# Kernel optimization log

Hardware: AMD Instinct MI355X
Metric: run time of the kernel (lower is better)

Reference implementation:

```python
import jax, jax.numpy as jnp
import numpy as np

MIN_TAU = 1e-3  # max(1e-5, config.CELL_MIN_TAU=0.001)
EPS_U = 1e-10   # guard for log(u) in gumbel transform


def setup_inputs() -> dict:
    key = jax.random.key(0)
    ks = jax.random.split(key, 6)
    B, I, H = 16, 1024, 2048
    x_t = jax.random.normal(ks[0], (B, I), dtype=jnp.float32)
    h_prev = jax.random.normal(ks[1], (B, H), dtype=jnp.float32)
    W_ih_w = jax.random.normal(ks[2], (H, I), dtype=jnp.float32) * (1.0 / np.sqrt(I))
    W_ih_b = jax.random.normal(ks[3], (H,), dtype=jnp.float32) * 0.01
    W_hh = jax.random.normal(ks[4], (H, H), dtype=jnp.float32) * np.sqrt(2.0 / (H + H))  # xavier
    hh_mask = jnp.ones((H, H), dtype=jnp.float32)
    temperature = jnp.ones((1,), dtype=jnp.float32)
    gumbel_noise = jax.random.uniform(ks[5], (B, H, H), dtype=jnp.float32)  # U(0,1); transformed in reference
    return {"x_t": x_t, "h_prev": h_prev, "W_ih_w": W_ih_w, "W_ih_b": W_ih_b,
            "W_hh": W_hh, "hh_mask": hh_mask, "temperature": temperature,
            "gumbel_noise": gumbel_noise}


def reference(x_t, h_prev, W_ih_w, W_ih_b, W_hh, hh_mask, temperature, gumbel_noise):
    # tau = clamp(temperature, min=1e-3)
    tau = jnp.maximum(temperature[0], MIN_TAU)
    # input contribution: Linear(input_size, hidden_size)
    input_contrib = x_t @ W_ih_w.T + W_ih_b  # (B, H)
    # effective recurrent logits (H, H), broadcast over batch
    effective = (W_hh * hh_mask) / tau
    # gumbel-softmax with tau=1.0, soft (training mode): softmax(logits + g) over last dim
    g = -jnp.log(-jnp.log(gumbel_noise + EPS_U) + EPS_U)  # standard Gumbel(0,1)
    gumbel_samples = jax.nn.softmax(effective[None, :, :] + g, axis=2)  # (B, H, H)
    # contrib = einsum('boh,bh->bo')
    contrib = jnp.einsum('boh,bh->bo', gumbel_samples, h_prev)
    preact = input_contrib + contrib
    # default neuron plan: single tanh kernel over all hidden units
    h_next = jnp.tanh(preact)
    return h_next
```

## Files before the change

### kernel.cpp

```cpp
#include <hip/hip_runtime.h>
#include <math.h>

#define BB 16
#define II 1024
#define HH 2048

#define LN2f   0.69314718055994530942f
#define LOG2Ef 1.44269504088896340736f
#define EPSG   1e-10f

__device__ __forceinline__ void acc1(float u, float w, float mk, float h,
                                     float k, float& s, float& t) {
    float L1    = __log2f(u + EPSG);
    float inner = fmaf(L1, -LN2f, EPSG);
    float L2    = __log2f(inner);
    float e     = exp2f(fmaf(w * mk, k, -L2));
    s += e;
    t = fmaf(e, h, t);
}

__global__ __launch_bounds__(256, 6) void reservoir_cell_kernel(
    const float* __restrict__ x_t,
    const float* __restrict__ h_prev,
    const float* __restrict__ W_ih_w,
    const float* __restrict__ W_ih_b,
    const float* __restrict__ W_hh,
    const float* __restrict__ hh_mask,
    const float* __restrict__ temperature,
    const float* __restrict__ gumbel,
    float* __restrict__ out)
{
    const int n    = blockIdx.x;
    const int o    = ((n >> 5) << 3) + (n & 7);
    const int grp  = (n >> 3) & 3;
    const int wave = threadIdx.x >> 6;
    const int lane = threadIdx.x & 63;
    const int b    = (grp << 2) + wave;

    const float tau = fmaxf(temperature[0], 1e-3f);
    const float k   = LOG2Ef / tau;

    const float4* g4 = (const float4*)(gumbel + ((size_t)b * HH + o) * HH);
    const float4* h4 = (const float4*)(W_hh   + (size_t)o * HH);
    const float4* m4 = (const float4*)(hh_mask+ (size_t)o * HH);
    const float4* p4 = (const float4*)(h_prev + (size_t)b * HH);

    float s = 0.0f, t = 0.0f;
    #pragma unroll
    for (int j = 0; j < 8; ++j) {
        float4 u  = g4[j * 64 + lane];
        float4 w  = h4[j * 64 + lane];
        float4 mk = m4[j * 64 + lane];
        float4 hv = p4[j * 64 + lane];
        acc1(u.x, w.x, mk.x, hv.x, k, s, t);
        acc1(u.y, w.y, mk.y, hv.y, k, s, t);
        acc1(u.z, w.z, mk.z, hv.z, k, s, t);
        acc1(u.w, w.w, mk.w, hv.w, k, s, t);
    }
    #pragma unroll
    for (int off = 32; off; off >>= 1) {
        s += __shfl_down(s, off, 64);
        t += __shfl_down(t, off, 64);
    }

    const float4* x4 = (const float4*)(x_t + (size_t)b * II);
    const float4* w4 = (const float4*)(W_ih_w + (size_t)o * II);
    float ic = 0.0f;
    #pragma unroll
    for (int j = 0; j < 4; ++j) {
        float4 xv = x4[j * 64 + lane];
        float4 wv = w4[j * 64 + lane];
        ic += xv.x * wv.x + xv.y * wv.y + xv.z * wv.z + xv.w * wv.w;
    }
    #pragma unroll
    for (int off = 32; off; off >>= 1) ic += __shfl_down(ic, off, 64);

    if (lane == 0) {
        out[(size_t)b * HH + o] = tanhf(ic + W_ih_b[o] + t / s);
    }
}

extern "C" void kernel_launch(void* const* d_in, const int* in_sizes, int n_in,
                              void* d_out, int out_size, void* d_ws, size_t ws_size,
                              hipStream_t stream) {
    const float* x_t         = (const float*)d_in[0];
    const float* h_prev      = (const float*)d_in[1];
    const float* W_ih_w      = (const float*)d_in[2];
    const float* W_ih_b      = (const float*)d_in[3];
    const float* W_hh        = (const float*)d_in[4];
    const float* hh_mask     = (const float*)d_in[5];
    const float* temperature = (const float*)d_in[6];
    const float* gumbel      = (const float*)d_in[7];
    float* out = (float*)d_out;

    dim3 grid(8192), block(256);
    reservoir_cell_kernel<<<grid, block, 0, stream>>>(
        x_t, h_prev, W_ih_w, W_ih_b, W_hh, hh_mask, temperature, gumbel, out);
}
```

Measured before the change: 403.2 us.

## Stage scaled W_hh*mask row in shared memory and stream gumbel with nontemporal loads

```diff
diff --git a/kernel.cpp b/kernel.cpp
--- a/kernel.cpp
+++ b/kernel.cpp
@@ -9,15 +9,7 @@
 #define LOG2Ef 1.44269504088896340736f
 #define EPSG   1e-10f
 
-__device__ __forceinline__ void acc1(float u, float w, float mk, float h,
-                                     float k, float& s, float& t) {
-    float L1    = __log2f(u + EPSG);
-    float inner = fmaf(L1, -LN2f, EPSG);
-    float L2    = __log2f(inner);
-    float e     = exp2f(fmaf(w * mk, k, -L2));
-    s += e;
-    t = fmaf(e, h, t);
-}
+typedef float nt_f4 __attribute__((ext_vector_type(4)));
 
 __global__ __launch_bounds__(256, 6) void reservoir_cell_kernel(
     const float* __restrict__ x_t,
@@ -33,47 +25,70 @@
     const int n    = blockIdx.x;
     const int o    = ((n >> 5) << 3) + (n & 7);
     const int grp  = (n >> 3) & 3;
-    const int wave = threadIdx.x >> 6;
-    const int lane = threadIdx.x & 63;
+    const int tid  = threadIdx.x;
+    const int lane = tid & 63;
+    const int wave = tid >> 6;
     const int b    = (grp << 2) + wave;
 
     const float tau = fmaxf(temperature[0], 1e-3f);
     const float k   = LOG2Ef / tau;
 
-    const float4* g4 = (const float4*)(gumbel + ((size_t)b * HH + o) * HH);
-    const float4* h4 = (const float4*)(W_hh   + (size_t)o * HH);
-    const float4* m4 = (const float4*)(hh_mask+ (size_t)o * HH);
+    __shared__ float4 wmk4[HH / 4];
+
+    const float4* wrow = (const float4*)(W_hh    + (size_t)o * HH);
+    const float4* mrow = (const float4*)(hh_mask + (size_t)o * HH);
+    float4 w0 = wrow[tid], w1 = wrow[tid + 256];
+    float4 q0 = mrow[tid], q1 = mrow[tid + 256];
+
+    const float4* x4 = (const float4*)(x_t    + (size_t)b * II);
+    const float4* v4 = (const float4*)(W_ih_w + (size_t)o * II);
+    float ic = 0.0f;
+    #pragma unroll
+    for (int j = 0; j < 4; ++j) {
+        float4 xv = x4[j * 64 + lane];
+        float4 wv = v4[j * 64 + lane];
+        ic += xv.x * wv.x + xv.y * wv.y + xv.z * wv.z + xv.w * wv.w;
+    }
+
+    float4 r0, r1;
+    r0.x = w0.x * q0.x * k; r0.y = w0.y * q0.y * k;
+    r0.z = w0.z * q0.z * k; r0.w = w0.w * q0.w * k;
+    r1.x = w1.x * q1.x * k; r1.y = w1.y * q1.y * k;
+    r1.z = w1.z * q1.z * k; r1.w = w1.w * q1.w * k;
+    wmk4[tid] = r0;
+    wmk4[tid + 256] = r1;
+    __syncthreads();
+
+    const nt_f4*  g4 = (const nt_f4*)(gumbel + ((size_t)b * HH + o) * HH);
     const float4* p4 = (const float4*)(h_prev + (size_t)b * HH);
 
     float s = 0.0f, t = 0.0f;
     #pragma unroll
     for (int j = 0; j < 8; ++j) {
-        float4 u  = g4[j * 64 + lane];
-        float4 w  = h4[j * 64 + lane];
-        float4 mk = m4[j * 64 + lane];
+        nt_f4  u  = __builtin_nontemporal_load(&g4[j * 64 + lane]);
         float4 hv = p4[j * 64 + lane];
-        acc1(u.x, w.x, mk.x, hv.x, k, s, t);
-        acc1(u.y, w.y, mk.y, hv.y, k, s, t);
-        acc1(u.z, w.z, mk.z, hv.z, k, s, t);
-        acc1(u.w, w.w, mk.w, hv.w, k, s, t);
+        float4 wm = wmk4[j * 64 + lane];
+        float L1, inner, L2, e;
+
+        L1 = __log2f(u.x + EPSG); inner = fmaf(L1, -LN2f, EPSG);
+        L2 = __log2f(inner); e = exp2f(wm.x - L2); s += e; t = fmaf(e, hv.x, t);
+
+        L1 = __log2f(u.y + EPSG); inner = fmaf(L1, -LN2f, EPSG);
+        L2 = __log2f(inner); e = exp2f(wm.y - L2); s += e; t = fmaf(e, hv.y, t);
+
+        L1 = __log2f(u.z + EPSG); inner = fmaf(L1, -LN2f, EPSG);
+        L2 = __log2f(inner); e = exp2f(wm.z - L2); s += e; t = fmaf(e, hv.z, t);
+
+        L1 = __log2f(u.w + EPSG); inner = fmaf(L1, -LN2f, EPSG);
+        L2 = __log2f(inner); e = exp2f(wm.w - L2); s += e; t = fmaf(e, hv.w, t);
     }
+
     #pragma unroll
     for (int off = 32; off; off >>= 1) {
-        s += __shfl_down(s, off, 64);
-        t += __shfl_down(t, off, 64);
+        s  += __shfl_down(s,  off, 64);
+        t  += __shfl_down(t,  off, 64);
+        ic += __shfl_down(ic, off, 64);
     }
-
-    const float4* x4 = (const float4*)(x_t + (size_t)b * II);
-    const float4* w4 = (const float4*)(W_ih_w + (size_t)o * II);
-    float ic = 0.0f;
-    #pragma unroll
-    for (int j = 0; j < 4; ++j) {
-        float4 xv = x4[j * 64 + lane];
-        float4 wv = w4[j * 64 + lane];
-        ic += xv.x * wv.x + xv.y * wv.y + xv.z * wv.z + xv.w * wv.w;
-    }
-    #pragma unroll
-    for (int off = 32; off; off >>= 1) ic += __shfl_down(ic, off, 64);
 
     if (lane == 0) {
         out[(size_t)b * HH + o] = tanhf(ic + W_ih_b[o] + t / s);
```

Measured after the change: 391.4 us. -2.9%, faster.
